# Performance work log

Hardware: AMD Instinct MI355X
Metric: run time of the kernel (lower is better)

The kernel has to match this reference:

```python
import jax, jax.numpy as jnp
import numpy as np

EMBED_DIM = 512
N_HEADS = 8
HEAD_DIM = EMBED_DIM // N_HEADS
SEQ = 4096
BATCH = 2


def setup_inputs() -> dict:
    key = jax.random.key(0)
    k1, k2, k3 = jax.random.split(key, 3)
    x = jax.random.normal(k1, (SEQ, BATCH, EMBED_DIM), dtype=jnp.float32)
    # xavier_uniform for [3E, E]: limit = sqrt(6/(3E+E))
    lim_in = float(np.sqrt(6.0 / (3 * EMBED_DIM + EMBED_DIM)))
    in_proj_weight = jax.random.uniform(k2, (3 * EMBED_DIM, EMBED_DIM), minval=-lim_in, maxval=lim_in, dtype=jnp.float32)
    in_proj_bias = jnp.zeros((3 * EMBED_DIM,), jnp.float32)
    lim_out = float(np.sqrt(1.0 / EMBED_DIM))  # torch Linear default init range
    out_weight = jax.random.uniform(k3, (EMBED_DIM, EMBED_DIM), minval=-lim_out, maxval=lim_out, dtype=jnp.float32)
    out_bias = jnp.zeros((EMBED_DIM,), jnp.float32)
    return {"x": x, "in_proj_weight": in_proj_weight, "in_proj_bias": in_proj_bias,
            "out_weight": out_weight, "out_bias": out_bias}


def reference(x, in_proj_weight, in_proj_bias, out_weight, out_bias):
    # x: [S, B, E] (seq-first, as in the torch module)
    S, B, E = x.shape
    H, D = N_HEADS, HEAD_DIM
    scaling = 1.0 / (D ** 0.5)
    qkv = x @ in_proj_weight.T + in_proj_bias            # [S, B, 3E]
    q, k, v = jnp.split(qkv, 3, axis=-1)                 # each [S, B, E]
    # reshape to [B*H, S, D]
    def to_bh(t):
        return t.reshape(S, B * H, D).transpose(1, 0, 2)
    q = to_bh(q * scaling)
    k = to_bh(k)
    v = to_bh(v)
    scores = jnp.einsum('bqd,bkd->bqk', q, k)            # [B*H, S, S]
    attn = jax.nn.softmax(scores, axis=-1)
    out = jnp.einsum('bqk,bkd->bqd', attn, v)            # [B*H, S, D]
    out = out.transpose(1, 0, 2).reshape(S, B, E)        # [S, B, E]
    return out @ out_weight.T + out_bias
```

## Files before the change

### kernel.cpp

```cpp
#include <hip/hip_runtime.h>

typedef unsigned short u16;
typedef unsigned int   u32;
typedef short bf16x8 __attribute__((ext_vector_type(8)));
typedef float f32x2  __attribute__((ext_vector_type(2)));
typedef float f32x4  __attribute__((ext_vector_type(4)));
typedef float f32x16 __attribute__((ext_vector_type(16)));
typedef u32   u32x4  __attribute__((ext_vector_type(4)));

#define QK_SCALE 0.18033688011112042f

__device__ __forceinline__ u16 f2bf(float f) {
  u32 u = __builtin_bit_cast(u32, f);
  u = (u + 0x7FFFu + ((u >> 16) & 1u)) >> 16;
  return (u16)u;
}

__device__ __forceinline__ u32 cvtpk(float lo, float hi) {
  u32 r;
  asm("v_cvt_pk_bf16_f32 %0, %1, %2" : "=v"(r) : "v"(lo), "v"(hi));
  return r;
}

__device__ __forceinline__ void gload16(void* lds, const void* g) {
  __builtin_amdgcn_global_load_lds(
      (const __attribute__((address_space(1))) u32*)g,
      (__attribute__((address_space(3))) u32*)lds, 16, 0, 0);
}

__device__ __forceinline__ bf16x8 ld8(const void* p) {
  return *(const bf16x8*)p;
}

__device__ __forceinline__ f32x16 fz16() { f32x16 z = {}; return z; }

__global__ __launch_bounds__(256) void cvt_kernel(
    const float* __restrict__ x, const float* __restrict__ w1,
    const float* __restrict__ w2,
    u16* __restrict__ xb, u16* __restrict__ wb, u16* __restrict__ ob) {
  int i = blockIdx.x * 256 + threadIdx.x;
  const float* src; u16* dst; int off;
  if (i < 1048576)            { src = x;  dst = xb; off = i; }
  else if (i < 1048576+196608){ src = w1; dst = wb; off = i - 1048576; }
  else                        { src = w2; dst = ob; off = i - 1245184; }
  float4 v = ((const float4*)src)[off];
  ushort4 o;
  o.x = f2bf(v.x); o.y = f2bf(v.y); o.z = f2bf(v.z); o.w = f2bf(v.w);
  ((ushort4*)dst)[off] = o;
}

template<int MODE>
__global__ __launch_bounds__(256, 2) void gemm_bt(
    const u16* __restrict__ A, const u16* __restrict__ Bm,
    const float* __restrict__ bias,
    u16* __restrict__ q_out, u16* __restrict__ k_out, u16* __restrict__ v_out,
    float* __restrict__ f_out, int M, int N, int K) {
  __shared__ __attribute__((aligned(16))) u16 As[128 * 64];
  __shared__ __attribute__((aligned(16))) u16 Bs[128 * 64];
  const int tid = threadIdx.x, lane = tid & 63, w = tid >> 6;
  const int wm = w >> 1, wn = w & 1;
  const int lo = lane & 15, hi = lane >> 4;
  const int m0 = blockIdx.x * 128, n0 = blockIdx.y * 128;
  f32x4 acc[4][4] = {};
  const int srow = lane >> 3;
  const int skc  = (lane & 7) ^ srow;
  const int nk = K >> 6;
  for (int kt = 0; kt < nk; ++kt) {
    __syncthreads();
    const int k0 = kt * 64;
#pragma unroll
    for (int c = 0; c < 4; ++c) {
      const int ch = w * 4 + c;
      const int row = ch * 8 + srow;
      gload16((char*)As + ch * 1024, A  + (size_t)(m0 + row) * K + k0 + skc * 8);
      gload16((char*)Bs + ch * 1024, Bm + (size_t)(n0 + row) * K + k0 + skc * 8);
    }
    __syncthreads();
#pragma unroll
    for (int kk = 0; kk < 2; ++kk) {
      bf16x8 af[4], bfr[4];
#pragma unroll
      for (int mi = 0; mi < 4; ++mi) {
        const int row = wm * 64 + mi * 16 + lo;
        const int kc = kk * 4 + hi;
        af[mi] = ld8((const char*)As + row * 128 + ((kc ^ (row & 7)) << 4));
      }
#pragma unroll
      for (int ni = 0; ni < 4; ++ni) {
        const int row = wn * 64 + ni * 16 + lo;
        const int kc = kk * 4 + hi;
        bfr[ni] = ld8((const char*)Bs + row * 128 + ((kc ^ (row & 7)) << 4));
      }
#pragma unroll
      for (int mi = 0; mi < 4; ++mi)
#pragma unroll
        for (int ni = 0; ni < 4; ++ni)
          acc[mi][ni] = __builtin_amdgcn_mfma_f32_16x16x32_bf16(
              af[mi], bfr[ni], acc[mi][ni], 0, 0, 0);
    }
  }
#pragma unroll
  for (int mi = 0; mi < 4; ++mi)
#pragma unroll
    for (int ni = 0; ni < 4; ++ni) {
      const int gn = n0 + wn * 64 + ni * 16 + lo;
      const float bv = bias[gn];
#pragma unroll
      for (int r = 0; r < 4; ++r) {
        const int gm = m0 + wm * 64 + mi * 16 + hi * 4 + r;
        float val = acc[mi][ni][r] + bv;
        if (MODE == 0) {
          const int s = gm >> 1, b = gm & 1;
          const int sec = gn >> 9, e = gn & 511;
          const int h = e >> 6, d = e & 63;
          const size_t o = (((size_t)(b * 8 + h) * 4096 + s) << 6) + d;
          if (sec == 0)      q_out[o] = f2bf(val * QK_SCALE);
          else if (sec == 1) k_out[o] = f2bf(val);
          else               v_out[o] = f2bf(val);
        } else {
          f_out[(size_t)gm * N + gn] = val;
        }
      }
    }
}

__global__ __launch_bounds__(256) void transpose_v(
    const u16* __restrict__ v, u16* __restrict__ vt) {
  __shared__ __attribute__((aligned(16))) u16 T[64 * 72];
  const int bh = blockIdx.y, s0 = blockIdx.x * 64;
  const int t = threadIdx.x;
#pragma unroll
  for (int i = 0; i < 2; ++i) {
    const int idx = t + i * 256;
    const int row = idx >> 3, c = idx & 7;
    uint4 d = *(const uint4*)(v + ((size_t)bh * 4096 + s0 + row) * 64 + c * 8);
    *(uint4*)(&T[row * 72 + c * 8]) = d;
  }
  __syncthreads();
#pragma unroll
  for (int i = 0; i < 2; ++i) {
    const int idx = t + i * 256;
    const int dcol = idx >> 3, sc = idx & 7;
    u16 tmp[8];
#pragma unroll
    for (int j = 0; j < 8; ++j) tmp[j] = T[(sc * 8 + j) * 72 + dcol];
    *(uint4*)(vt + ((size_t)bh * 64 + dcol) * 4096 + s0 + sc * 8) = *(const uint4*)tmp;
  }
}

__global__ __launch_bounds__(256, 2) void fa_kernel(
    const u16* __restrict__ q, const u16* __restrict__ k,
    const u16* __restrict__ vt, u16* __restrict__ attn) {
  __shared__ __attribute__((aligned(16))) char S_lds[2][2][16384];
  __shared__ float Ml[2][32];
  const int tid = threadIdx.x, lane = tid & 63, w = tid >> 6;
  const int lo = lane & 31, hi5 = lane >> 5;
  const int wq = w & 1;
  const int kvh = w >> 1;
  const int wg = blockIdx.x;
  const int xcd = wg & 7, idx = wg >> 3;
  const int bh = xcd * 2 + (idx >> 6), qb = idx & 63;
  const int q0 = qb * 64 + wq * 32;
  const size_t hb = (size_t)bh * 4096 * 64;
  const u16* kbase = k + hb;
  const u16* vbase = vt + hb;
  bf16x8 qf[4];
#pragma unroll
  for (int ds = 0; ds < 4; ++ds)
    qf[ds] = ld8(q + hb + (size_t)(q0 + lo) * 64 + ds * 16 + hi5 * 8);

  f32x16 acc[2] = {};
  float lrun = 0.f;
  f32x16 stE0, stE1, stO0, stO1;
  bf16x8 vfE[8], vfO[8];

  const int srow8 = lane >> 3;
  const int sx    = (lane & 7) ^ srow8;
  const int schunk = wq * 4;

#define STAGE(buf, kv0)                                                       \
  {                                                                           \
    char* kb_l = S_lds[kvh][buf];                                             \
    char* vb_l = kb_l + 8192;                                                 \
    _Pragma("unroll")                                                         \
    for (int i = 0; i < 4; ++i) {                                             \
      const int c = schunk + i;                       \
      gload16(kb_l + c * 1024,                                                \
              kbase + (size_t)((kv0) + c * 8 + srow8) * 64 + sx * 8);         \
      gload16(vb_l + c * 1024,                                                \
              vbase + (size_t)(c * 8 + srow8) * 4096 + (kv0) + sx * 8);       \
    }                                                                         \
  }

#define PACK(stv, ksl, pa)                                                    \
  {                                                                           \
    u32 A0 = cvtpk(stv[8 * ksl + 0], stv[8 * ksl + 1]);                       \
    u32 A1 = cvtpk(stv[8 * ksl + 2], stv[8 * ksl + 3]);                       \
    u32 B0 = cvtpk(stv[8 * ksl + 4], stv[8 * ksl + 5]);                       \
    u32 B1 = cvtpk(stv[8 * ksl + 6], stv[8 * ksl + 7]);                       \
    asm("v_permlane32_swap_b32 %0, %1" : "+v"(A0), "+v"(B0));                 \
    asm("v_permlane32_swap_b32 %0, %1" : "+v"(A1), "+v"(B1));                 \
    u32x4 pw; pw.x = A0; pw.y = A1; pw.z = B0; pw.w = B1;                     \
    pa = __builtin_bit_cast(bf16x8, pw);                                      \
  }

#define PRODUCE(CUR, S0, S1, VF)                                              \
  {                                                                           \
    const char* kl = S_lds[kvh][CUR];                                         \
    const char* vl = kl + 8192;                                               \
    S0 = fz16(); S1 = fz16();                                                 \
    _Pragma("unroll")                                                         \
    for (int ds = 0; ds < 4; ++ds) {                                          \
      const int r0 = lo, r1 = 32 + lo;                                        \
      const int col = ds * 32 + hi5 * 16;                                     \
      bf16x8 kf0 = ld8(kl + r0 * 128 + (col ^ ((r0 & 7) << 4)));              \
      bf16x8 kf1 = ld8(kl + r1 * 128 + (col ^ ((r1 & 7) << 4)));              \
      S0 = __builtin_amdgcn_mfma_f32_32x32x16_bf16(kf0, qf[ds], S0, 0, 0, 0); \
      S1 = __builtin_amdgcn_mfma_f32_32x32x16_bf16(kf1, qf[ds], S1, 0, 0, 0); \
    }                                                                         \
    _Pragma("unroll")                                                         \
    for (int sl = 0; sl < 4; ++sl)                                            \
      _Pragma("unroll")                                                       \
      for (int ds2 = 0; ds2 < 2; ++ds2) {                                     \
        const int row = ds2 * 32 + lo;                                        \
        VF[sl * 2 + ds2] = ld8(vl + row * 128 +                               \
                               ((sl * 32 + hi5 * 16) ^ ((row & 7) << 4)));    \
      }                                                                       \
  }

#define CONSUME(S0, S1, VF)                                                   \
  {                                                                           \
    f32x2 lt; lt.x = 0.f; lt.y = 0.f;                                         \
    _Pragma("unroll")                                                         \
    for (int i = 0; i < 8; ++i) {                                             \
      S0[2*i]   = __builtin_amdgcn_exp2f(S0[2*i]);                            \
      S0[2*i+1] = __builtin_amdgcn_exp2f(S0[2*i+1]);                          \
      f32x2 e0; e0.x = S0[2*i]; e0.y = S0[2*i+1]; lt += e0;                   \
      S1[2*i]   = __builtin_amdgcn_exp2f(S1[2*i]);                            \
      S1[2*i+1] = __builtin_amdgcn_exp2f(S1[2*i+1]);                          \
      f32x2 e1; e1.x = S1[2*i]; e1.y = S1[2*i+1]; lt += e1;                   \
    }                                                                         \
    lrun += lt.x + lt.y;                                                      \
    bf16x8 pa0, pa1, pa2, pa3;                                                \
    PACK(S0, 0, pa0); PACK(S0, 1, pa1);                                       \
    PACK(S1, 0, pa2); PACK(S1, 1, pa3);                                       \
    __builtin_amdgcn_s_setprio(1);                                            \
    _Pragma("unroll")                                                         \
    for (int ds2 = 0; ds2 < 2; ++ds2) {                                       \
      acc[ds2] = __builtin_amdgcn_mfma_f32_32x32x16_bf16(pa0, VF[0 + ds2],    \
                                                         acc[ds2], 0, 0, 0); \
      acc[ds2] = __builtin_amdgcn_mfma_f32_32x32x16_bf16(pa1, VF[2 + ds2],    \
                                                         acc[ds2], 0, 0, 0); \
      acc[ds2] = __builtin_amdgcn_mfma_f32_32x32x16_bf16(pa2, VF[4 + ds2],    \
                                                         acc[ds2], 0, 0, 0); \
      acc[ds2] = __builtin_amdgcn_mfma_f32_32x32x16_bf16(pa3, VF[6 + ds2],    \
                                                         acc[ds2], 0, 0, 0); \
    }                                                                         \
    __builtin_amdgcn_s_setprio(0);                                            \
  }

  const int kvbase = kvh * 2048;
  STAGE(0, kvbase);
  __syncthreads();
  STAGE(1, kvbase + 64);
  PRODUCE(0, stE0, stE1, vfE);
  __syncthreads();

  for (int t = 1; t < 31; t += 2) {
    STAGE(0, kvbase + (t + 1) * 64);
    PRODUCE(1, stO0, stO1, vfO);
    CONSUME(stE0, stE1, vfE);
    __syncthreads();
    STAGE(1, kvbase + (t + 2) * 64);
    PRODUCE(0, stE0, stE1, vfE);
    CONSUME(stO0, stO1, vfO);
    __syncthreads();
  }
  PRODUCE(1, stO0, stO1, vfO);
  CONSUME(stE0, stE1, vfE);
  CONSUME(stO0, stO1, vfO);

  lrun += __shfl_xor(lrun, 32);
  __syncthreads();
  float* Ob = (float*)S_lds;
  if (w >= 2) {
#pragma unroll
    for (int r = 0; r < 16; ++r) {
      const int crow = (r & 3) + 8 * (r >> 2) + 4 * hi5;
#pragma unroll
      for (int ds2 = 0; ds2 < 2; ++ds2)
        Ob[(wq * 32 + crow) * 64 + ds2 * 32 + lo] = acc[ds2][r];
    }
    if (hi5 == 0) Ml[wq][lo] = lrun;
  }
  __syncthreads();
  if (w < 2) {
    const float linv = 1.0f / (lrun + Ml[wq][lo]);
    const int b = bh >> 3, h = bh & 7;
#pragma unroll
    for (int r = 0; r < 16; ++r) {
      const int crow = (r & 3) + 8 * (r >> 2) + 4 * hi5;
      const float ivR = __shfl(linv, crow);
      const int s = q0 + crow;
#pragma unroll
      for (int ds2 = 0; ds2 < 2; ++ds2) {
        const float ob = Ob[(wq * 32 + crow) * 64 + ds2 * 32 + lo];
        attn[(size_t)(s * 2 + b) * 512 + h * 64 + ds2 * 32 + lo] =
            f2bf((acc[ds2][r] + ob) * ivR);
      }
    }
  }
#undef STAGE
#undef PACK
#undef PRODUCE
#undef CONSUME
}

extern "C" void kernel_launch(void* const* d_in, const int* in_sizes, int n_in,
                              void* d_out, int out_size, void* d_ws, size_t ws_size,
                              hipStream_t stream) {
  const float* x     = (const float*)d_in[0];
  const float* w_in  = (const float*)d_in[1];
  const float* b_in  = (const float*)d_in[2];
  const float* w_out = (const float*)d_in[3];
  const float* b_out = (const float*)d_in[4];
  float* out = (float*)d_out;
  char* ws = (char*)d_ws;
  u16* xb  = (u16*)(ws);
  u16* wb  = (u16*)(ws + 8388608);
  u16* ob  = (u16*)(ws + 9961472);
  u16* qb  = (u16*)(ws + 10485760);
  u16* kb  = (u16*)(ws + 18874368);
  u16* vb  = (u16*)(ws + 27262976);
  u16* vtb = (u16*)(ws + 35651584);
  u16* attn = xb;

  cvt_kernel<<<5120, 256, 0, stream>>>(x, w_in, w_out, xb, wb, ob);
  gemm_bt<0><<<dim3(64, 12), 256, 0, stream>>>(xb, wb, b_in, qb, kb, vb,
                                               nullptr, 8192, 1536, 512);
  transpose_v<<<dim3(64, 16), 256, 0, stream>>>(vb, vtb);
  fa_kernel<<<1024, 256, 0, stream>>>(qb, kb, vtb, attn);
  gemm_bt<1><<<dim3(64, 4), 256, 0, stream>>>(attn, ob, b_out, nullptr, nullptr,
                                              nullptr, out, 8192, 512, 512);
}
```

Baseline: 139.2 us.

## Restructure flash-attention pipeline to single V buffer and raise occupancy to 3

Splits the shared-memory staging into double-buffered K and a single-buffered V, which cuts LDS per block from 64KB to 48KB. The software pipeline is rewritten: the score tile is packed to bf16 right away and held in registers, so only one set of score and V fragments stays live. The old pipeline kept two score sets (even and odd) in flight. Launch bounds move from 2 to 3 blocks per CU to use the lower register and LDS pressure for more occupancy. In exchange, the V load now serialises with the V read through an extra barrier each iteration, and there is less overlap between the QK and PV matrix ops.

```diff
diff --git a/kernel.cpp b/kernel.cpp
--- a/kernel.cpp
+++ b/kernel.cpp
@@ -148,10 +148,11 @@
   }
 }
 
-__global__ __launch_bounds__(256, 2) void fa_kernel(
+__global__ __launch_bounds__(256, 3) void fa_kernel(
     const u16* __restrict__ q, const u16* __restrict__ k,
     const u16* __restrict__ vt, u16* __restrict__ attn) {
-  __shared__ __attribute__((aligned(16))) char S_lds[2][2][16384];
+  __shared__ __attribute__((aligned(16))) char K_lds[2][2][8192];
+  __shared__ __attribute__((aligned(16))) char V_lds[2][8192];
   __shared__ float Ml[2][32];
   const int tid = threadIdx.x, lane = tid & 63, w = tid >> 6;
   const int lo = lane & 31, hi5 = lane >> 5;
@@ -171,28 +172,46 @@
 
   f32x16 acc[2] = {};
   float lrun = 0.f;
-  f32x16 stE0, stE1, stO0, stO1;
-  bf16x8 vfE[8], vfO[8];
+  bf16x8 pa[4];
+  bf16x8 vfr[8];
 
   const int srow8 = lane >> 3;
   const int sx    = (lane & 7) ^ srow8;
   const int schunk = wq * 4;
 
-#define STAGE(buf, kv0)                                                       \
-  {                                                                           \
-    char* kb_l = S_lds[kvh][buf];                                             \
-    char* vb_l = kb_l + 8192;                                                 \
+#define STAGE_K(buf, kv0)                                                     \
+  {                                                                           \
+    char* kb_l = K_lds[kvh][buf];                                             \
     _Pragma("unroll")                                                         \
     for (int i = 0; i < 4; ++i) {                                             \
       const int c = schunk + i;                       \
       gload16(kb_l + c * 1024,                                                \
               kbase + (size_t)((kv0) + c * 8 + srow8) * 64 + sx * 8);         \
+    }                                                                         \
+  }
+#define STAGE_V(kv0)                                                          \
+  {                                                                           \
+    char* vb_l = V_lds[kvh];                                                  \
+    _Pragma("unroll")                                                         \
+    for (int i = 0; i < 4; ++i) {                                             \
+      const int c = schunk + i;                                               \
       gload16(vb_l + c * 1024,                                                \
               vbase + (size_t)(c * 8 + srow8) * 4096 + (kv0) + sx * 8);       \
     }                                                                         \
   }
-
-#define PACK(stv, ksl, pa)                                                    \
+#define VREAD()                                                               \
+  {                                                                           \
+    const char* vl = V_lds[kvh];                                              \
+    _Pragma("unroll")                                                         \
+    for (int sl = 0; sl < 4; ++sl)                                            \
+      _Pragma("unroll")                                                       \
+      for (int ds2 = 0; ds2 < 2; ++ds2) {                                     \
+        const int row = ds2 * 32 + lo;                                        \
+        vfr[sl * 2 + ds2] = ld8(vl + row * 128 +                              \
+                                ((sl * 32 + hi5 * 16) ^ ((row & 7) << 4)));   \
+      }                                                                       \
+  }
+#define PACK(stv, ksl, dst)                                                   \
   {                                                                           \
     u32 A0 = cvtpk(stv[8 * ksl + 0], stv[8 * ksl + 1]);                       \
     u32 A1 = cvtpk(stv[8 * ksl + 2], stv[8 * ksl + 3]);                       \
@@ -201,14 +220,24 @@
     asm("v_permlane32_swap_b32 %0, %1" : "+v"(A0), "+v"(B0));                 \
     asm("v_permlane32_swap_b32 %0, %1" : "+v"(A1), "+v"(B1));                 \
     u32x4 pw; pw.x = A0; pw.y = A1; pw.z = B0; pw.w = B1;                     \
-    pa = __builtin_bit_cast(bf16x8, pw);                                      \
-  }
-
-#define PRODUCE(CUR, S0, S1, VF)                                              \
-  {                                                                           \
-    const char* kl = S_lds[kvh][CUR];                                         \
-    const char* vl = kl + 8192;                                               \
+    dst = __builtin_bit_cast(bf16x8, pw);                                     \
+  }
+#define PVSTEP()                                                              \
+  {                                                                           \
+    __builtin_amdgcn_s_setprio(1);                                            \
+    _Pragma("unroll")                                                         \
+    for (int sl = 0; sl < 4; ++sl)                                            \
+      _Pragma("unroll")                                                       \
+      for (int ds2 = 0; ds2 < 2; ++ds2)                                       \
+        acc[ds2] = __builtin_amdgcn_mfma_f32_32x32x16_bf16(                   \
+            pa[sl], vfr[sl * 2 + ds2], acc[ds2], 0, 0, 0);                    \
+    __builtin_amdgcn_s_setprio(0);                                            \
+  }
+#define QKSTEP(CUR, S0, S1)                                                   \
+  {                                                                           \
+    const char* kl = K_lds[kvh][CUR];                                         \
     S0 = fz16(); S1 = fz16();                                                 \
+    __builtin_amdgcn_s_setprio(1);                                            \
     _Pragma("unroll")                                                         \
     for (int ds = 0; ds < 4; ++ds) {                                          \
       const int r0 = lo, r1 = 32 + lo;                                        \
@@ -218,17 +247,9 @@
       S0 = __builtin_amdgcn_mfma_f32_32x32x16_bf16(kf0, qf[ds], S0, 0, 0, 0); \
       S1 = __builtin_amdgcn_mfma_f32_32x32x16_bf16(kf1, qf[ds], S1, 0, 0, 0); \
     }                                                                         \
-    _Pragma("unroll")                                                         \
-    for (int sl = 0; sl < 4; ++sl)                                            \
-      _Pragma("unroll")                                                       \
-      for (int ds2 = 0; ds2 < 2; ++ds2) {                                     \
-        const int row = ds2 * 32 + lo;                                        \
-        VF[sl * 2 + ds2] = ld8(vl + row * 128 +                               \
-                               ((sl * 32 + hi5 * 16) ^ ((row & 7) << 4)));    \
-      }                                                                       \
-  }
-
-#define CONSUME(S0, S1, VF)                                                   \
+    __builtin_amdgcn_s_setprio(0);                                            \
+  }
+#define SMPACK(S0, S1)                                                        \
   {                                                                           \
     f32x2 lt; lt.x = 0.f; lt.y = 0.f;                                         \
     _Pragma("unroll")                                                         \
@@ -241,48 +262,41 @@
       f32x2 e1; e1.x = S1[2*i]; e1.y = S1[2*i+1]; lt += e1;                   \
     }                                                                         \
     lrun += lt.x + lt.y;                                                      \
-    bf16x8 pa0, pa1, pa2, pa3;                                                \
-    PACK(S0, 0, pa0); PACK(S0, 1, pa1);                                       \
-    PACK(S1, 0, pa2); PACK(S1, 1, pa3);                                       \
-    __builtin_amdgcn_s_setprio(1);                                            \
-    _Pragma("unroll")                                                         \
-    for (int ds2 = 0; ds2 < 2; ++ds2) {                                       \
-      acc[ds2] = __builtin_amdgcn_mfma_f32_32x32x16_bf16(pa0, VF[0 + ds2],    \
-                                                         acc[ds2], 0, 0, 0); \
-      acc[ds2] = __builtin_amdgcn_mfma_f32_32x32x16_bf16(pa1, VF[2 + ds2],    \
-                                                         acc[ds2], 0, 0, 0); \
-      acc[ds2] = __builtin_amdgcn_mfma_f32_32x32x16_bf16(pa2, VF[4 + ds2],    \
-                                                         acc[ds2], 0, 0, 0); \
-      acc[ds2] = __builtin_amdgcn_mfma_f32_32x32x16_bf16(pa3, VF[6 + ds2],    \
-                                                         acc[ds2], 0, 0, 0); \
-    }                                                                         \
-    __builtin_amdgcn_s_setprio(0);                                            \
+    PACK(S0, 0, pa[0]); PACK(S0, 1, pa[1]);                                   \
+    PACK(S1, 0, pa[2]); PACK(S1, 1, pa[3]);                                   \
   }
 
   const int kvbase = kvh * 2048;
-  STAGE(0, kvbase);
-  __syncthreads();
-  STAGE(1, kvbase + 64);
-  PRODUCE(0, stE0, stE1, vfE);
-  __syncthreads();
-
-  for (int t = 1; t < 31; t += 2) {
-    STAGE(0, kvbase + (t + 1) * 64);
-    PRODUCE(1, stO0, stO1, vfO);
-    CONSUME(stE0, stE1, vfE);
+  f32x16 st0, st1;
+  STAGE_K(0, kvbase);
+  STAGE_V(kvbase);
+  __syncthreads();
+  VREAD();
+  __syncthreads();
+  STAGE_K(1, kvbase + 64);
+  STAGE_V(kvbase + 64);
+  QKSTEP(0, st0, st1);
+  SMPACK(st0, st1);
+  __syncthreads();
+
+  for (int t = 1; t < 32; ++t) {
+    const int cur = t & 1;
+    PVSTEP();
+    VREAD();
     __syncthreads();
-    STAGE(1, kvbase + (t + 2) * 64);
-    PRODUCE(0, stE0, stE1, vfE);
-    CONSUME(stO0, stO1, vfO);
+    if (t < 31) {
+      STAGE_K(cur ^ 1, kvbase + (t + 1) * 64);
+      STAGE_V(kvbase + (t + 1) * 64);
+    }
+    QKSTEP(cur, st0, st1);
+    SMPACK(st0, st1);
     __syncthreads();
   }
-  PRODUCE(1, stO0, stO1, vfO);
-  CONSUME(stE0, stE1, vfE);
-  CONSUME(stO0, stO1, vfO);
+  PVSTEP();
 
   lrun += __shfl_xor(lrun, 32);
   __syncthreads();
-  float* Ob = (float*)S_lds;
+  float* Ob = (float*)K_lds;
   if (w >= 2) {
 #pragma unroll
     for (int r = 0; r < 16; ++r) {
@@ -310,10 +324,13 @@
       }
     }
   }
-#undef STAGE
+#undef STAGE_K
+#undef STAGE_V
+#undef VREAD
 #undef PACK
-#undef PRODUCE
-#undef CONSUME
+#undef PVSTEP
+#undef QKSTEP
+#undef SMPACK
 }
 
 extern "C" void kernel_launch(void* const* d_in, const int* in_sizes, int n_in,
```

Measured after the change: 149.7 us. +7.5%, slower.
